# Performance work log

Hardware: AMD Instinct MI355X
Metric: run time of the kernel (lower is better)

Reference implementation:

```python
import jax, jax.numpy as jnp
import numpy as np

N_NODES = 100000
N_EDGES = 3200000
N_SG = 800000  # edges in the softmax-normalized segment
RULES = 9

SUB_MAT = np.array([[-0.2, -0.1, -0.05, -0.05, -0.05, -0.01, -0.055, -0.01, 0.0],
                    [0.0, -0.002, -0.001, -0.001, -0.001, -0.0002, 0.0008, -0.0002, 0.0]], dtype=np.float32)
SUB_BIAS = np.array([1, 0.7, 0.275, 0.4, 0.25, 0.07, 0.2225, 0.07, 0], dtype=np.float32)


def setup_inputs() -> dict:
    key = jax.random.key(0)
    k1, k2, k3 = jax.random.split(key, 3)
    feat = jax.random.normal(k1, (N_NODES, 4), dtype=jnp.float32)
    src = jax.random.randint(k2, (N_EDGES,), 0, N_NODES)
    dst = jax.random.randint(k3, (N_EDGES,), 0, N_NODES)
    edge_sg_ID = jnp.arange(N_SG, dtype=jnp.int64 if jax.config.read('jax_enable_x64') else jnp.int32).reshape(1, N_SG)
    return {
        'feat': feat,
        'src': src,
        'dst': dst,
        'edge_sg_ID': edge_sg_ID,
        'sub_systems_mat': jnp.asarray(SUB_MAT),
        'sub_systems_bias': jnp.asarray(SUB_BIAS),
    }


def _gauss(x, mean, sigma):
    return jnp.exp(-(x - mean) ** 2 / (2.0 * sigma ** 2))


def _ante_generator(vector):
    # vector: [E, 4] = (dpos_x, dpos_y, dvel_x, dvel_y)
    d = vector[:, :2]
    v = vector[:, 2:]
    x1 = jnp.linalg.norm(d, axis=1, keepdims=True)  # distance, [E,1]
    vnorm = jnp.linalg.norm(v, axis=1, keepdims=True)
    cos = jnp.sum(d * v, axis=1, keepdims=True) / (x1 * vnorm + 1e-8)
    x2 = jnp.degrees(jnp.arccos(jnp.clip(cos, -1.0 + 1e-6, 1.0 - 1e-6)))  # angle deg, [E,1]
    return x1, x2


def _ante_process(x1, x2):
    # memberships: x1 small/med/large, x2 small/med/large
    m1 = [_gauss(x1, 0.0, 0.75), _gauss(x1, 2.0, 0.75), _gauss(x1, 4.0, 0.75)]
    m2 = [_gauss(x2, 0.0, 30.0), _gauss(x2, 90.0, 30.0), _gauss(x2, 180.0, 30.0)]
    # 9 rules: min over all (x1_level, x2_level) pairs -> [E, 1, 9]
    return jnp.stack([jnp.minimum(a, b) for a in m1 for b in m2], axis=2)


def _forward(feat, sub_systems_mat, sub_systems_bias, src, dst, edge_sg_ID):
    vector = feat[dst] - feat[src]  # [E, 4]
    x1, x2 = _ante_generator(vector)  # each [E, 1]
    truth = _ante_process(x1, x2)  # [E, 1, 9]
    premises = jnp.stack((x1, x2), axis=2).reshape(-1, 2)  # [E, 2]
    consequence = premises @ sub_systems_mat + sub_systems_bias  # [E, 9]
    consequence = consequence.reshape(x1.shape[0], x1.shape[1], RULES)  # [E, 1, 9]
    attention = jnp.sum(truth * consequence, axis=2) / jnp.sum(truth, axis=2)  # [E, 1]
    attention = attention[:, :, None]  # [E, 1, 1]
    idx = edge_sg_ID[0]
    # segment softmax over the selected edges (dim 0)
    attention = attention.at[idx].set(jax.nn.softmax(attention[idx], axis=0))
    return attention


def reference(feat, src, dst, edge_sg_ID, sub_systems_mat, sub_systems_bias):
    return _forward(feat, sub_systems_mat, sub_systems_bias, src, dst, edge_sg_ID)
```

## Files before the change

kernel.cpp:

```cpp
#include <hip/hip_runtime.h>

#define N_NODES 100000
#define N_EDGES 3200000
#define N_SG    800000
#define RULES   9
#define BLOCK   256
#define EPT     8
#define K1_THREADS (N_EDGES / EPT)
#define K1_BLOCKS  ((K1_THREADS + BLOCK - 1) / BLOCK)
#define SG_VEC     (N_SG / 4)
#define K2_BLOCKS  ((SG_VEC + BLOCK - 1) / BLOCK)


__device__ __forceinline__ float fast_acos_deg(float x)
{
    float ax = fabsf(x);
    float p = fmaf(ax, -0.0187293f, 0.0742610f);
    p = fmaf(p, ax, -0.2121144f);
    p = fmaf(p, ax, 1.5707288f);
    float r = __builtin_amdgcn_sqrtf(1.0f - ax) * p;
    r = (x < 0.0f) ? (3.14159265358979f - r) : r;
    return r * 57.29577951308232f;
}

__device__ __forceinline__ float edge_attn(float4 fd, float4 fs,
                                           const float* c1, const float* c2,
                                           const float* cb)
{
    float d0 = fd.x - fs.x, d1 = fd.y - fs.y;
    float v0 = fd.z - fs.z, v1 = fd.w - fs.w;

    float d2  = fmaf(d0, d0, d1 * d1);
    float v2  = fmaf(v0, v0, v1 * v1);
    float x1  = __builtin_amdgcn_sqrtf(d2);
    float dot = fmaf(d0, v0, d1 * v1);
    float cosv = dot * __builtin_amdgcn_rcpf(
                     __builtin_amdgcn_sqrtf(d2 * v2) + 1e-8f);
    cosv = fminf(fmaxf(cosv, -1.0f + 1e-6f), 1.0f - 1e-6f);
    float x2 = fast_acos_deg(cosv);

    const float k1 = 0.888888888888889f;
    const float k2 = 5.555555555555556e-4f;
    float m1[3], m2[3];
    float a;
    a = x1;          m1[0] = __expf(-a * a * k1);
    a = x1 - 2.0f;   m1[1] = __expf(-a * a * k1);
    a = x1 - 4.0f;   m1[2] = __expf(-a * a * k1);
    a = x2;          m2[0] = __expf(-a * a * k2);
    a = x2 - 90.0f;  m2[1] = __expf(-a * a * k2);
    a = x2 - 180.0f; m2[2] = __expf(-a * a * k2);

    float num = 0.0f, den = 0.0f;
#pragma unroll
    for (int i = 0; i < 3; ++i) {
#pragma unroll
        for (int j = 0; j < 3; ++j) {
            int r = i * 3 + j;
            float t = fminf(m1[i], m2[j]);
            float c = fmaf(x1, c1[r], fmaf(x2, c2[r], cb[r]));
            num = fmaf(t, c, num);
            den += t;
        }
    }
    return num * __builtin_amdgcn_rcpf(den);
}

__global__ __launch_bounds__(BLOCK, 4) void edge_attn_kernel(
    const float4* __restrict__ feat,
    const int4*   __restrict__ src4,
    const int4*   __restrict__ dst4,
    const float*  __restrict__ M,
    const float*  __restrict__ B,
    float4*       __restrict__ out4,
    float*        __restrict__ partials)
{
    int t = blockIdx.x * BLOCK + threadIdx.x;
    float s = 0.0f;

    if (t < K1_THREADS) {
        int4 sa = src4[2 * t], sb = src4[2 * t + 1];
        int4 da = dst4[2 * t], db = dst4[2 * t + 1];

        float4 fs0 = feat[sa.x], fs1 = feat[sa.y], fs2 = feat[sa.z], fs3 = feat[sa.w];
        float4 fs4 = feat[sb.x], fs5 = feat[sb.y], fs6 = feat[sb.z], fs7 = feat[sb.w];
        float4 fd0 = feat[da.x], fd1 = feat[da.y], fd2 = feat[da.z], fd3 = feat[da.w];
        float4 fd4 = feat[db.x], fd5 = feat[db.y], fd6 = feat[db.z], fd7 = feat[db.w];

        float c1[RULES], c2[RULES], cb[RULES];
#pragma unroll
        for (int r = 0; r < RULES; ++r) {
            c1[r] = M[r];
            c2[r] = M[RULES + r];
            cb[r] = B[r];
        }

        float4 ra, rb;
        ra.x = edge_attn(fd0, fs0, c1, c2, cb);
        ra.y = edge_attn(fd1, fs1, c1, c2, cb);
        ra.z = edge_attn(fd2, fs2, c1, c2, cb);
        ra.w = edge_attn(fd3, fs3, c1, c2, cb);
        rb.x = edge_attn(fd4, fs4, c1, c2, cb);
        rb.y = edge_attn(fd5, fs5, c1, c2, cb);
        rb.z = edge_attn(fd6, fs6, c1, c2, cb);
        rb.w = edge_attn(fd7, fs7, c1, c2, cb);
        out4[2 * t]     = ra;
        out4[2 * t + 1] = rb;

        if (t < N_SG / EPT) {
            s = __expf(ra.x) + __expf(ra.y) + __expf(ra.z) + __expf(ra.w)
              + __expf(rb.x) + __expf(rb.y) + __expf(rb.z) + __expf(rb.w);
        }
    }

#pragma unroll
    for (int o = 32; o > 0; o >>= 1) s += __shfl_down(s, o, 64);
    __shared__ float wsum[BLOCK / 64];
    if ((threadIdx.x & 63) == 0) wsum[threadIdx.x >> 6] = s;
    __syncthreads();
    if (threadIdx.x == 0)
        partials[blockIdx.x] = wsum[0] + wsum[1] + wsum[2] + wsum[3];
}

__global__ __launch_bounds__(BLOCK) void softmax_write_kernel(
    const float* __restrict__ partials,
    float4*      __restrict__ out4)
{
    float s = 0.0f;
    for (int p = threadIdx.x; p < K1_BLOCKS; p += BLOCK) s += partials[p];
#pragma unroll
    for (int o = 32; o > 0; o >>= 1) s += __shfl_down(s, o, 64);
    __shared__ float wsum[BLOCK / 64];
    if ((threadIdx.x & 63) == 0) wsum[threadIdx.x >> 6] = s;
    __syncthreads();
    float inv = 1.0f / (wsum[0] + wsum[1] + wsum[2] + wsum[3]);

    int i = blockIdx.x * BLOCK + threadIdx.x;
    if (i < SG_VEC) {
        float4 v = out4[i];
        v.x = __expf(v.x) * inv;
        v.y = __expf(v.y) * inv;
        v.z = __expf(v.z) * inv;
        v.w = __expf(v.w) * inv;
        out4[i] = v;
    }
}

extern "C" void kernel_launch(void* const* d_in, const int* in_sizes, int n_in,
                              void* d_out, int out_size, void* d_ws, size_t ws_size,
                              hipStream_t stream)
{
    const float4* feat = (const float4*)d_in[0];
    const int4*   src4 = (const int4*)d_in[1];
    const int4*   dst4 = (const int4*)d_in[2];
    const float*  M    = (const float*)d_in[4];
    const float*  B    = (const float*)d_in[5];
    float4* out4     = (float4*)d_out;
    float*  partials = (float*)d_ws;

    edge_attn_kernel<<<dim3(K1_BLOCKS), dim3(BLOCK), 0, stream>>>(
        feat, src4, dst4, M, B, out4, partials);
    softmax_write_kernel<<<dim3(K2_BLOCKS), dim3(BLOCK), 0, stream>>>(
        partials, out4);
}
```

Measured before the change: 117.0 us.

## Use fixed grid with remainder groups, nontemporal streams, and precomputed softmax exps

The edge kernel now launches a fixed grid of 1536 blocks, one full wave at 4 blocks/CU on 256 CUs. Each block handles 8 edges per thread plus a few leftover 4-edge groups on its first 9 threads. Index loads and non-softmax output stores use nontemporal hints to keep streaming data out of the cache. The softmax segment now stores exp(attention) directly, so the second kernel only multiplies by the inverse sum over a grid-stride loop with fewer blocks. The goal is to reduce tail effects and cache pollution and to remove duplicate exp work, at the cost of a slightly unbalanced remainder path.

```diff
diff --git a/kernel.cpp b/kernel.cpp
--- a/kernel.cpp
+++ b/kernel.cpp
@@ -5,11 +5,19 @@
 #define N_SG    800000
 #define RULES   9
 #define BLOCK   256
-#define EPT     8
-#define K1_THREADS (N_EDGES / EPT)
-#define K1_BLOCKS  ((K1_THREADS + BLOCK - 1) / BLOCK)
-#define SG_VEC     (N_SG / 4)
-#define K2_BLOCKS  ((SG_VEC + BLOCK - 1) / BLOCK)
+
+#define K1_BLOCKS    1536
+#define K1_THREADS   (K1_BLOCKS * BLOCK)
+#define MAIN_GROUPS  (K1_THREADS * 2)
+#define TOT_GROUPS   (N_EDGES / 4)
+#define REM_GROUPS   (TOT_GROUPS - MAIN_GROUPS)
+#define REM_PER_BLK  9
+#define SG_GROUPS    (N_SG / 4)
+#define SOFT_THREADS (N_SG / 8)
+#define K2_BLOCKS    768
+
+typedef float vf4 __attribute__((ext_vector_type(4)));
+typedef int   vi4 __attribute__((ext_vector_type(4)));
 
 
 __device__ __forceinline__ float fast_acos_deg(float x)
@@ -23,7 +31,7 @@
     return r * 57.29577951308232f;
 }
 
-__device__ __forceinline__ float edge_attn(float4 fd, float4 fs,
+__device__ __forceinline__ float edge_attn(vf4 fd, vf4 fs,
                                            const float* c1, const float* c2,
                                            const float* cb)
 {
@@ -66,49 +74,72 @@
 }
 
 __global__ __launch_bounds__(BLOCK, 4) void edge_attn_kernel(
-    const float4* __restrict__ feat,
-    const int4*   __restrict__ src4,
-    const int4*   __restrict__ dst4,
-    const float*  __restrict__ M,
-    const float*  __restrict__ B,
-    float4*       __restrict__ out4,
-    float*        __restrict__ partials)
+    const vf4*  __restrict__ feat,
+    const vi4*  __restrict__ src4,
+    const vi4*  __restrict__ dst4,
+    const float* __restrict__ M,
+    const float* __restrict__ B,
+    vf4*        __restrict__ out4,
+    float*      __restrict__ partials)
 {
-    int t = blockIdx.x * BLOCK + threadIdx.x;
+    const int T = blockIdx.x * BLOCK + threadIdx.x;
+
+    float c1[RULES], c2[RULES], cb[RULES];
+#pragma unroll
+    for (int r = 0; r < RULES; ++r) {
+        c1[r] = M[r];
+        c2[r] = M[RULES + r];
+        cb[r] = B[r];
+    }
+
+    vi4 sa = __builtin_nontemporal_load(&src4[2 * T]);
+    vi4 sb = __builtin_nontemporal_load(&src4[2 * T + 1]);
+    vi4 da = __builtin_nontemporal_load(&dst4[2 * T]);
+    vi4 db = __builtin_nontemporal_load(&dst4[2 * T + 1]);
+
+    vf4 fs0 = feat[sa.x], fs1 = feat[sa.y], fs2 = feat[sa.z], fs3 = feat[sa.w];
+    vf4 fs4 = feat[sb.x], fs5 = feat[sb.y], fs6 = feat[sb.z], fs7 = feat[sb.w];
+    vf4 fd0 = feat[da.x], fd1 = feat[da.y], fd2 = feat[da.z], fd3 = feat[da.w];
+    vf4 fd4 = feat[db.x], fd5 = feat[db.y], fd6 = feat[db.z], fd7 = feat[db.w];
+
+    vf4 ra, rb;
+    ra.x = edge_attn(fd0, fs0, c1, c2, cb);
+    ra.y = edge_attn(fd1, fs1, c1, c2, cb);
+    ra.z = edge_attn(fd2, fs2, c1, c2, cb);
+    ra.w = edge_attn(fd3, fs3, c1, c2, cb);
+    rb.x = edge_attn(fd4, fs4, c1, c2, cb);
+    rb.y = edge_attn(fd5, fs5, c1, c2, cb);
+    rb.z = edge_attn(fd6, fs6, c1, c2, cb);
+    rb.w = edge_attn(fd7, fs7, c1, c2, cb);
+
     float s = 0.0f;
+    if (T < SOFT_THREADS) {
+        ra.x = __expf(ra.x); ra.y = __expf(ra.y);
+        ra.z = __expf(ra.z); ra.w = __expf(ra.w);
+        rb.x = __expf(rb.x); rb.y = __expf(rb.y);
+        rb.z = __expf(rb.z); rb.w = __expf(rb.w);
+        s = (ra.x + ra.y + ra.z + ra.w) + (rb.x + rb.y + rb.z + rb.w);
+        out4[2 * T]     = ra;
+        out4[2 * T + 1] = rb;
+    } else {
+        __builtin_nontemporal_store(ra, &out4[2 * T]);
+        __builtin_nontemporal_store(rb, &out4[2 * T + 1]);
+    }
 
-    if (t < K1_THREADS) {
-        int4 sa = src4[2 * t], sb = src4[2 * t + 1];
-        int4 da = dst4[2 * t], db = dst4[2 * t + 1];
-
-        float4 fs0 = feat[sa.x], fs1 = feat[sa.y], fs2 = feat[sa.z], fs3 = feat[sa.w];
-        float4 fs4 = feat[sb.x], fs5 = feat[sb.y], fs6 = feat[sb.z], fs7 = feat[sb.w];
-        float4 fd0 = feat[da.x], fd1 = feat[da.y], fd2 = feat[da.z], fd3 = feat[da.w];
-        float4 fd4 = feat[db.x], fd5 = feat[db.y], fd6 = feat[db.z], fd7 = feat[db.w];
-
-        float c1[RULES], c2[RULES], cb[RULES];
-#pragma unroll
-        for (int r = 0; r < RULES; ++r) {
-            c1[r] = M[r];
-            c2[r] = M[RULES + r];
-            cb[r] = B[r];
-        }
-
-        float4 ra, rb;
-        ra.x = edge_attn(fd0, fs0, c1, c2, cb);
-        ra.y = edge_attn(fd1, fs1, c1, c2, cb);
-        ra.z = edge_attn(fd2, fs2, c1, c2, cb);
-        ra.w = edge_attn(fd3, fs3, c1, c2, cb);
-        rb.x = edge_attn(fd4, fs4, c1, c2, cb);
-        rb.y = edge_attn(fd5, fs5, c1, c2, cb);
-        rb.z = edge_attn(fd6, fs6, c1, c2, cb);
-        rb.w = edge_attn(fd7, fs7, c1, c2, cb);
-        out4[2 * t]     = ra;
-        out4[2 * t + 1] = rb;
-
-        if (t < N_SG / EPT) {
-            s = __expf(ra.x) + __expf(ra.y) + __expf(ra.z) + __expf(ra.w)
-              + __expf(rb.x) + __expf(rb.y) + __expf(rb.z) + __expf(rb.w);
+    if (threadIdx.x < REM_PER_BLK) {
+        int e = blockIdx.x * REM_PER_BLK + threadIdx.x;
+        if (e < REM_GROUPS) {
+            int g = MAIN_GROUPS + e;
+            vi4 sr = __builtin_nontemporal_load(&src4[g]);
+            vi4 dr = __builtin_nontemporal_load(&dst4[g]);
+            vf4 gs0 = feat[sr.x], gs1 = feat[sr.y], gs2 = feat[sr.z], gs3 = feat[sr.w];
+            vf4 gd0 = feat[dr.x], gd1 = feat[dr.y], gd2 = feat[dr.z], gd3 = feat[dr.w];
+            vf4 rr;
+            rr.x = edge_attn(gd0, gs0, c1, c2, cb);
+            rr.y = edge_attn(gd1, gs1, c1, c2, cb);
+            rr.z = edge_attn(gd2, gs2, c1, c2, cb);
+            rr.w = edge_attn(gd3, gs3, c1, c2, cb);
+            __builtin_nontemporal_store(rr, &out4[g]);
         }
     }
 
@@ -123,9 +154,10 @@
 
 __global__ __launch_bounds__(BLOCK) void softmax_write_kernel(
     const float* __restrict__ partials,
-    float4*      __restrict__ out4)
+    vf4*         __restrict__ out4)
 {
     float s = 0.0f;
+#pragma unroll
     for (int p = threadIdx.x; p < K1_BLOCKS; p += BLOCK) s += partials[p];
 #pragma unroll
     for (int o = 32; o > 0; o >>= 1) s += __shfl_down(s, o, 64);
@@ -134,13 +166,10 @@
     __syncthreads();
     float inv = 1.0f / (wsum[0] + wsum[1] + wsum[2] + wsum[3]);
 
-    int i = blockIdx.x * BLOCK + threadIdx.x;
-    if (i < SG_VEC) {
-        float4 v = out4[i];
-        v.x = __expf(v.x) * inv;
-        v.y = __expf(v.y) * inv;
-        v.z = __expf(v.z) * inv;
-        v.w = __expf(v.w) * inv;
+    for (int i = blockIdx.x * BLOCK + threadIdx.x; i < SG_GROUPS;
+         i += K2_BLOCKS * BLOCK) {
+        vf4 v = out4[i];
+        v.x *= inv; v.y *= inv; v.z *= inv; v.w *= inv;
         out4[i] = v;
     }
 }
@@ -149,13 +178,13 @@
                               void* d_out, int out_size, void* d_ws, size_t ws_size,
                               hipStream_t stream)
 {
-    const float4* feat = (const float4*)d_in[0];
-    const int4*   src4 = (const int4*)d_in[1];
-    const int4*   dst4 = (const int4*)d_in[2];
-    const float*  M    = (const float*)d_in[4];
-    const float*  B    = (const float*)d_in[5];
-    float4* out4     = (float4*)d_out;
-    float*  partials = (float*)d_ws;
+    const vf4*   feat = (const vf4*)d_in[0];
+    const vi4*   src4 = (const vi4*)d_in[1];
+    const vi4*   dst4 = (const vi4*)d_in[2];
+    const float* M    = (const float*)d_in[4];
+    const float* B    = (const float*)d_in[5];
+    vf4*   out4     = (vf4*)d_out;
+    float* partials = (float*)d_ws;
 
     edge_attn_kernel<<<dim3(K1_BLOCKS), dim3(BLOCK), 0, stream>>>(
         feat, src4, dst4, M, B, out4, partials);
```

After: 118.9 us. No clear change (+1.6%).
